# Kernel tuning notes

Hardware: AMD Instinct MI355X
Metric: run time of the kernel (lower is better)

The kernel has to match this reference:

```python
import jax, jax.numpy as jnp
import numpy as np


def _gcn_conv(x, W, b, src, dst, deg_inv_sqrt, n_nodes):
    # x: [N, Fin], W: [Fin, Fout]; edges (with self-loops): src, dst [E+N]
    h = x @ W  # [N, Fout]
    norm = deg_inv_sqrt[src] * deg_inv_sqrt[dst]  # [E+N]
    msgs = h[src] * norm[:, None]  # gather-multiply
    out = jax.ops.segment_sum(msgs, dst, num_segments=n_nodes)  # scatter-add
    return out + b


def setup_inputs() -> dict:
    key = jax.random.key(0)
    k1, k2, k3, k4 = jax.random.split(key, 4)
    N, E, FIN, HID, OUT = 100000, 3200000, 128, 32, 32
    x = jax.random.normal(k1, (N, FIN), dtype=jnp.float32)
    edge_index = jax.random.randint(k2, (2, E), 0, N, dtype=jnp.int64)
    W1 = jax.random.normal(k3, (FIN, HID), dtype=jnp.float32) * (1.0 / np.sqrt(FIN))
    b1 = jnp.zeros((HID,), dtype=jnp.float32)
    W2 = jax.random.normal(k4, (HID, OUT), dtype=jnp.float32) * (1.0 / np.sqrt(HID))
    b2 = jnp.zeros((OUT,), dtype=jnp.float32)
    return {"x": x, "edge_index": edge_index, "W1": W1, "b1": b1, "W2": W2, "b2": b2}


def reference(x, edge_index, W1, b1, W2, b2):
    n = x.shape[0]
    # GCNConv defaults: add self-loops, symmetric normalization D^-1/2 (A+I) D^-1/2
    loops = jnp.arange(n, dtype=edge_index.dtype)
    src = jnp.concatenate([edge_index[0], loops])
    dst = jnp.concatenate([edge_index[1], loops])
    deg = jax.ops.segment_sum(jnp.ones_like(dst, dtype=x.dtype), dst, num_segments=n)
    deg_inv_sqrt = jnp.where(deg > 0, jax.lax.rsqrt(jnp.maximum(deg, 1.0)), 0.0)
    h = jax.nn.relu(_gcn_conv(x, W1, b1, src, dst, deg_inv_sqrt, n))  # hidden layer + ReLU
    out = jax.nn.relu(_gcn_conv(h, W2, b2, src, dst, deg_inv_sqrt, n))  # last layer + last_activation relu
    return out
```

## Files before the change

kernel.cpp:

```cpp
#include <hip/hip_runtime.h>
#include <hip/hip_fp16.h>

#define FIN 128
#define HID 32
#define BSHIFT 8
#define BNODES 256
#define CHUNK 2048
#define NBMAX 512
#define CAPB 8960
#define G1ROWS 64
#define XPAD 4


__global__ __launch_bounds__(256) void chunk_sort_kernel(const int* __restrict__ src,
                                                         const int* __restrict__ dst,
                                                         int* __restrict__ ec,
                                                         unsigned short* __restrict__ offt,
                                                         int E, int nb) {
    __shared__ int hist[NBMAX];
    __shared__ int pref[NBMAX];
    __shared__ int wsum[128];
    __shared__ int sorted[CHUNK];
    int c = blockIdx.x, t = threadIdx.x;
    int beg = c * CHUNK;
    int cnt = min(CHUNK, E - beg);
    for (int i = t; i < nb; i += 256) hist[i] = 0;
    __syncthreads();
    int bk[8], ent[8];
    #pragma unroll
    for (int j = 0; j < 8; ++j) {
        int i = t + j * 256;
        if (i < cnt) {
            int d = dst[beg + i];
            bk[j]  = ((unsigned)d) >> BSHIFT;
            ent[j] = src[beg + i] | ((d & (BNODES - 1)) << 24);
            atomicAdd(&hist[bk[j]], 1);
        } else bk[j] = -1;
    }
    __syncthreads();
    if (t < 128) {
        int s = 0;
        #pragma unroll
        for (int j = 0; j < 4; ++j) {
            int idx = t * 4 + j;
            int v = (idx < nb) ? hist[idx] : 0;
            pref[idx] = s; s += v;
        }
        wsum[t] = s;
    }
    __syncthreads();
    if (t == 0) { int run = 0; for (int j = 0; j < 128; ++j) { int v = wsum[j]; wsum[j] = run; run += v; } }
    __syncthreads();
    for (int i = t; i < nb; i += 256) { int p = pref[i] + wsum[i >> 2]; pref[i] = p; hist[i] = p; }
    __syncthreads();
    #pragma unroll
    for (int j = 0; j < 8; ++j) {
        if (bk[j] >= 0) {
            int p = atomicAdd(&hist[bk[j]], 1);
            sorted[p] = ent[j];
        }
    }
    __syncthreads();
    for (int i = t; i < cnt; i += 256) ec[(size_t)c * CHUNK + i] = sorted[i];
    unsigned short* row = offt + (size_t)c * (nb + 1);
    for (int i = t; i < nb; i += 256) row[i] = (unsigned short)pref[i];
    if (t == 0) row[nb] = (unsigned short)cnt;
}


__global__ __launch_bounds__(1024) void bucket_build_kernel(const int* __restrict__ ec,
                                                            const unsigned short* __restrict__ offt,
                                                            int* __restrict__ entries,
                                                            float* __restrict__ dinv,
                                                            int* __restrict__ rowbeg,
                                                            int* __restrict__ rowcnt,
                                                            int n, int nb, int nchunks, int cap) {
    __shared__ int raw[CAPB];
    __shared__ int srt[CAPB];
    __shared__ int hist[BNODES];
    __shared__ int pref[BNODES];
    __shared__ int cursor[BNODES];
    __shared__ int wsum[64];
    __shared__ int nfill;
    int b = blockIdx.x, t = threadIdx.x;
    if (t < BNODES) hist[t] = 0;
    if (t == 0) nfill = 0;
    __syncthreads();
    for (int c = t; c < nchunks; c += 1024) {
        const unsigned short* row = offt + (size_t)c * (nb + 1);
        int s = row[b], e2 = row[b + 1];
        int m = e2 - s;
        if (m > 0) {
            int base = atomicAdd(&nfill, m);
            const int* p = ec + (size_t)c * CHUNK + s;
            for (int k = 0; k < m; ++k) {
                int e = p[k];
                if (base + k < CAPB) raw[base + k] = e;
                atomicAdd(&hist[((unsigned)e) >> 24], 1);
            }
        }
    }
    __syncthreads();
    int total = min(nfill, CAPB);
    if (t < 64) {
        int s = 0;
        #pragma unroll
        for (int j = 0; j < 4; ++j) { int v = hist[t * 4 + j]; pref[t * 4 + j] = s; s += v; }
        wsum[t] = s;
    }
    __syncthreads();
    if (t == 0) { int run = 0; for (int j = 0; j < 64; ++j) { int v = wsum[j]; wsum[j] = run; run += v; } }
    __syncthreads();
    if (t < BNODES) { int p = pref[t] + wsum[t >> 2]; pref[t] = p; cursor[t] = p; }
    __syncthreads();
    for (int i = t; i < total; i += 1024) {
        int e = raw[i];
        int p = atomicAdd(&cursor[((unsigned)e) >> 24], 1);
        srt[p] = e;
    }
    __syncthreads();
    int* ep = entries + (size_t)b * cap;
    for (int i = t; i < total; i += 1024) ep[i] = srt[i];
    int node = b * BNODES + t;
    if (t < BNODES && node < n) {
        int deg = hist[t];
        dinv[node]   = rsqrtf((float)deg + 1.0f);
        rowbeg[node] = b * cap + pref[t];
        rowcnt[node] = deg;
    }
}


__global__ __launch_bounds__(256) void gemm1_kernel(const float* __restrict__ x,
                                                    const float* __restrict__ W,
                                                    const float* __restrict__ dinv,
                                                    __half* __restrict__ h16, int n) {
    __shared__ float Ws[FIN * HID];
    int t = threadIdx.x;
    for (int i = t; i < FIN * HID; i += 256) Ws[i] = W[i];
    __syncthreads();
    int row0 = blockIdx.x * G1ROWS;
    int tr = t >> 3, tc = t & 7;
    int r0 = row0 + tr * 2, c0 = tc * 4;
    bool v0 = r0 < n, v1 = (r0 + 1) < n;
    const float* p0 = v0 ? &x[(size_t)r0 * FIN] : x;
    const float* p1 = v1 ? &x[(size_t)(r0 + 1) * FIN] : x;
    float4 a0 = make_float4(0.f, 0.f, 0.f, 0.f);
    float4 a1 = make_float4(0.f, 0.f, 0.f, 0.f);
    #pragma unroll 8
    for (int k4 = 0; k4 < FIN / 4; ++k4) {
        float4 xv0 = *(const float4*)&p0[k4 * 4];
        float4 xv1 = *(const float4*)&p1[k4 * 4];
        float4 w0 = *(const float4*)&Ws[(k4 * 4 + 0) * HID + c0];
        float4 w1 = *(const float4*)&Ws[(k4 * 4 + 1) * HID + c0];
        float4 w2 = *(const float4*)&Ws[(k4 * 4 + 2) * HID + c0];
        float4 w3 = *(const float4*)&Ws[(k4 * 4 + 3) * HID + c0];
        a0.x = fmaf(xv0.x, w0.x, a0.x); a0.y = fmaf(xv0.x, w0.y, a0.y);
        a0.z = fmaf(xv0.x, w0.z, a0.z); a0.w = fmaf(xv0.x, w0.w, a0.w);
        a0.x = fmaf(xv0.y, w1.x, a0.x); a0.y = fmaf(xv0.y, w1.y, a0.y);
        a0.z = fmaf(xv0.y, w1.z, a0.z); a0.w = fmaf(xv0.y, w1.w, a0.w);
        a0.x = fmaf(xv0.z, w2.x, a0.x); a0.y = fmaf(xv0.z, w2.y, a0.y);
        a0.z = fmaf(xv0.z, w2.z, a0.z); a0.w = fmaf(xv0.z, w2.w, a0.w);
        a0.x = fmaf(xv0.w, w3.x, a0.x); a0.y = fmaf(xv0.w, w3.y, a0.y);
        a0.z = fmaf(xv0.w, w3.z, a0.z); a0.w = fmaf(xv0.w, w3.w, a0.w);
        a1.x = fmaf(xv1.x, w0.x, a1.x); a1.y = fmaf(xv1.x, w0.y, a1.y);
        a1.z = fmaf(xv1.x, w0.z, a1.z); a1.w = fmaf(xv1.x, w0.w, a1.w);
        a1.x = fmaf(xv1.y, w1.x, a1.x); a1.y = fmaf(xv1.y, w1.y, a1.y);
        a1.z = fmaf(xv1.y, w1.z, a1.z); a1.w = fmaf(xv1.y, w1.w, a1.w);
        a1.x = fmaf(xv1.z, w2.x, a1.x); a1.y = fmaf(xv1.z, w2.y, a1.y);
        a1.z = fmaf(xv1.z, w2.z, a1.z); a1.w = fmaf(xv1.z, w2.w, a1.w);
        a1.x = fmaf(xv1.w, w3.x, a1.x); a1.y = fmaf(xv1.w, w3.y, a1.y);
        a1.z = fmaf(xv1.w, w3.z, a1.z); a1.w = fmaf(xv1.w, w3.w, a1.w);
    }
    #pragma unroll
    for (int rr = 0; rr < 2; ++rr) {
        int row = r0 + rr;
        float4 a = rr ? a1 : a0;
        float sc = (row < n) ? dinv[row] : 0.f;
        __half2 q0 = __floats2half2_rn(a.x * sc, a.y * sc);
        __half2 q1 = __floats2half2_rn(a.z * sc, a.w * sc);
        __half2* dstp = (__half2*)&h16[(size_t)row * HID + c0];
        dstp[0] = q0;
        dstp[1] = q1;
    }
}


__global__ __launch_bounds__(256) void gather_kernel(const int* __restrict__ entries,
                                                     const int* __restrict__ rowbeg,
                                                     const int* __restrict__ rowcnt,
                                                     const float* __restrict__ dinv,
                                                     const __half* __restrict__ h16,
                                                     const float* __restrict__ bias,
                                                     float* __restrict__ out, int n, int sent) {
    int t = threadIdx.x;
    int g = t >> 4, f = t & 15;
    int i = blockIdx.x * 16 + g;
    if (i >= n) return;
    float di = dinv[i];
    float s0, s1;
    {
        __half2 h = *(const __half2*)&h16[(size_t)i * HID + f * 2];
        float2 fp = __half22float2(h);
        s0 = fp.x; s1 = fp.y;
    }
    int beg = rowbeg[i], cnt = rowcnt[i];
    for (int base = 0; base < cnt; base += 16) {
        int idx = beg + base + f;
        int sv = ((base + f) < cnt) ? entries[idx] : sent;
        sv &= 0xFFFFFF;
        #pragma unroll
        for (int j0 = 0; j0 < 16; j0 += 8) {
            __half2 hv[8];
            #pragma unroll
            for (int j = 0; j < 8; ++j) {
                int e = __shfl(sv, j0 + j, 16);
                hv[j] = *(const __half2*)&h16[(size_t)e * HID + f * 2];
            }
            #pragma unroll
            for (int j = 0; j < 8; ++j) {
                s0 += __half2float(__low2half(hv[j]));
                s1 += __half2float(__high2half(hv[j]));
            }
        }
    }
    float2 b2 = *(const float2*)&bias[f * 2];
    float2 o;
    o.x = fmaxf(b2.x + di * s0, 0.f);
    o.y = fmaxf(b2.y + di * s1, 0.f);
    *(float2*)&out[(size_t)i * HID + f * 2] = o;
}


__global__ __launch_bounds__(256) void gemm2_kernel(const float* __restrict__ hin,
                                                    const float* __restrict__ W,
                                                    const float* __restrict__ dinv,
                                                    __half* __restrict__ h16, int n) {
    __shared__ float Ws[HID * HID];
    __shared__ float hs[G1ROWS][HID + XPAD];
    int t = threadIdx.x;
    for (int i = t; i < HID * HID; i += 256) Ws[i] = W[i];
    int row0 = blockIdx.x * G1ROWS;
    for (int idx = t; idx < G1ROWS * (HID / 4); idx += 256) {
        int r  = idx >> 3;
        int c4 = (idx & 7) * 4;
        int row = row0 + r;
        float4 v = (row < n) ? *(const float4*)&hin[(size_t)row * HID + c4]
                             : make_float4(0.f, 0.f, 0.f, 0.f);
        *(float4*)&hs[r][c4] = v;
    }
    __syncthreads();
    int tr = t >> 3, tc = t & 7;
    int r0 = tr * 2, c0 = tc * 4;
    float4 a0 = make_float4(0.f, 0.f, 0.f, 0.f);
    float4 a1 = make_float4(0.f, 0.f, 0.f, 0.f);
    #pragma unroll
    for (int k4 = 0; k4 < HID / 4; ++k4) {
        float4 xv0 = *(const float4*)&hs[r0][k4 * 4];
        float4 xv1 = *(const float4*)&hs[r0 + 1][k4 * 4];
        float4 w0 = *(const float4*)&Ws[(k4 * 4 + 0) * HID + c0];
        float4 w1 = *(const float4*)&Ws[(k4 * 4 + 1) * HID + c0];
        float4 w2 = *(const float4*)&Ws[(k4 * 4 + 2) * HID + c0];
        float4 w3 = *(const float4*)&Ws[(k4 * 4 + 3) * HID + c0];
        a0.x = fmaf(xv0.x, w0.x, a0.x); a0.y = fmaf(xv0.x, w0.y, a0.y);
        a0.z = fmaf(xv0.x, w0.z, a0.z); a0.w = fmaf(xv0.x, w0.w, a0.w);
        a0.x = fmaf(xv0.y, w1.x, a0.x); a0.y = fmaf(xv0.y, w1.y, a0.y);
        a0.z = fmaf(xv0.y, w1.z, a0.z); a0.w = fmaf(xv0.y, w1.w, a0.w);
        a0.x = fmaf(xv0.z, w2.x, a0.x); a0.y = fmaf(xv0.z, w2.y, a0.y);
        a0.z = fmaf(xv0.z, w2.z, a0.z); a0.w = fmaf(xv0.z, w2.w, a0.w);
        a0.x = fmaf(xv0.w, w3.x, a0.x); a0.y = fmaf(xv0.w, w3.y, a0.y);
        a0.z = fmaf(xv0.w, w3.z, a0.z); a0.w = fmaf(xv0.w, w3.w, a0.w);
        a1.x = fmaf(xv1.x, w0.x, a1.x); a1.y = fmaf(xv1.x, w0.y, a1.y);
        a1.z = fmaf(xv1.x, w0.z, a1.z); a1.w = fmaf(xv1.x, w0.w, a1.w);
        a1.x = fmaf(xv1.y, w1.x, a1.x); a1.y = fmaf(xv1.y, w1.y, a1.y);
        a1.z = fmaf(xv1.y, w1.z, a1.z); a1.w = fmaf(xv1.y, w1.w, a1.w);
        a1.x = fmaf(xv1.z, w2.x, a1.x); a1.y = fmaf(xv1.z, w2.y, a1.y);
        a1.z = fmaf(xv1.z, w2.z, a1.z); a1.w = fmaf(xv1.z, w2.w, a1.w);
        a1.x = fmaf(xv1.w, w3.x, a1.x); a1.y = fmaf(xv1.w, w3.y, a1.y);
        a1.z = fmaf(xv1.w, w3.z, a1.z); a1.w = fmaf(xv1.w, w3.w, a1.w);
    }
    #pragma unroll
    for (int rr = 0; rr < 2; ++rr) {
        int row = row0 + r0 + rr;
        float4 a = rr ? a1 : a0;
        float sc = (row < n) ? dinv[row] : 0.f;
        __half2 q0 = __floats2half2_rn(a.x * sc, a.y * sc);
        __half2 q1 = __floats2half2_rn(a.z * sc, a.w * sc);
        __half2* dstp = (__half2*)&h16[(size_t)row * HID + c0];
        dstp[0] = q0;
        dstp[1] = q1;
    }
}

extern "C" void kernel_launch(void* const* d_in, const int* in_sizes, int n_in,
                              void* d_out, int out_size, void* d_ws, size_t ws_size,
                              hipStream_t stream) {
    const float* x  = (const float*)d_in[0];
    const int*   ei = (const int*)d_in[1];
    const float* W1 = (const float*)d_in[2];
    const float* b1 = (const float*)d_in[3];
    const float* W2 = (const float*)d_in[4];
    const float* b2 = (const float*)d_in[5];
    float* out = (float*)d_out;

    int n = in_sizes[0] / FIN;
    int E = in_sizes[1] / 2;
    const int* src = ei;
    const int* dst = ei + E;

    int nb = (n + BNODES - 1) / BNODES;
    int nchunks = (E + CHUNK - 1) / CHUNK;
    int ggrid = (n + G1ROWS) / G1ROWS;
    int npad = ggrid * G1ROWS;
    int cap = CAPB;

    char* ws = (char*)d_ws;
    size_t off = 0;
    auto alloc = [&](size_t bytes) { char* p = ws + off; off += (bytes + 255) & ~(size_t)255; return p; };
    int*            ec      = (int*)alloc((size_t)nchunks * CHUNK * 4);
    unsigned short* offt    = (unsigned short*)alloc((size_t)nchunks * (nb + 1) * 2);
    int*            entries = (int*)alloc((size_t)nb * cap * 4);
    float*          dinv    = (float*)alloc((size_t)n * 4);
    int*            rowbeg  = (int*)alloc((size_t)n * 4);
    int*            rowcnt  = (int*)alloc((size_t)n * 4);
    float*          acc     = (float*)alloc((size_t)n * HID * 4);
    __half*         hh      = (__half*)alloc((size_t)npad * HID * 2);

    chunk_sort_kernel<<<nchunks, 256, 0, stream>>>(src, dst, ec, offt, E, nb);
    bucket_build_kernel<<<nb, 1024, 0, stream>>>(ec, offt, entries, dinv, rowbeg, rowcnt,
                                                 n, nb, nchunks, cap);

    gemm1_kernel<<<ggrid, 256, 0, stream>>>(x, W1, dinv, hh, n);
    gather_kernel<<<(n + 15) / 16, 256, 0, stream>>>(entries, rowbeg, rowcnt, dinv, hh, b1, acc, n, n);

    gemm2_kernel<<<ggrid, 256, 0, stream>>>(acc, W2, dinv, hh, n);
    gather_kernel<<<(n + 15) / 16, 256, 0, stream>>>(entries, rowbeg, rowcnt, dinv, hh, b2, out, n, n);
}
```

Measured before the change: 250.7 us.

## Widen gather to 16-byte row loads and use wave-shuffle prefix scans

The gather kernel now maps 4 lanes per node, each loading 8 fp16 features as one 16-byte vector, instead of 16 lanes each loading a 4-byte half2. This cuts the number of memory transactions per neighbour row and raises nodes per block from 16 to 64. The prefix scans in the sort and bucket kernels are replaced by a single-wave shuffle scan, which removes a serial thread-0 loop and two barriers. The bucket fill loop is also unrolled by four. The trade-off is more registers per thread in the gather, and fewer lanes per node to hide latency on high-degree nodes.

```diff
diff --git a/kernel.cpp b/kernel.cpp
--- a/kernel.cpp
+++ b/kernel.cpp
@@ -19,7 +19,6 @@
                                                          int E, int nb) {
     __shared__ int hist[NBMAX];
     __shared__ int pref[NBMAX];
-    __shared__ int wsum[128];
     __shared__ int sorted[CHUNK];
     int c = blockIdx.x, t = threadIdx.x;
     int beg = c * CHUNK;
@@ -38,20 +37,28 @@
         } else bk[j] = -1;
     }
     __syncthreads();
-    if (t < 128) {
+    if (t < 64) {
+        int v[8];
         int s = 0;
         #pragma unroll
-        for (int j = 0; j < 4; ++j) {
-            int idx = t * 4 + j;
-            int v = (idx < nb) ? hist[idx] : 0;
-            pref[idx] = s; s += v;
-        }
-        wsum[t] = s;
-    }
-    __syncthreads();
-    if (t == 0) { int run = 0; for (int j = 0; j < 128; ++j) { int v = wsum[j]; wsum[j] = run; run += v; } }
-    __syncthreads();
-    for (int i = t; i < nb; i += 256) { int p = pref[i] + wsum[i >> 2]; pref[i] = p; hist[i] = p; }
+        for (int j = 0; j < 8; ++j) {
+            int idx = t * 8 + j;
+            int h = (idx < nb) ? hist[idx] : 0;
+            v[j] = s; s += h;
+        }
+        int run = s;
+        #pragma unroll
+        for (int d = 1; d < 64; d <<= 1) {
+            int o = __shfl_up(run, d, 64);
+            if (t >= d) run += o;
+        }
+        int excl = run - s;
+        #pragma unroll
+        for (int j = 0; j < 8; ++j) {
+            int idx = t * 8 + j;
+            if (idx < nb) { int p = excl + v[j]; pref[idx] = p; hist[idx] = p; }
+        }
+    }
     __syncthreads();
     #pragma unroll
     for (int j = 0; j < 8; ++j) {
@@ -80,7 +87,6 @@
     __shared__ int hist[BNODES];
     __shared__ int pref[BNODES];
     __shared__ int cursor[BNODES];
-    __shared__ int wsum[64];
     __shared__ int nfill;
     int b = blockIdx.x, t = threadIdx.x;
     if (t < BNODES) hist[t] = 0;
@@ -93,7 +99,19 @@
         if (m > 0) {
             int base = atomicAdd(&nfill, m);
             const int* p = ec + (size_t)c * CHUNK + s;
-            for (int k = 0; k < m; ++k) {
+            int k = 0;
+            for (; k + 4 <= m; k += 4) {
+                int e0 = p[k], e1 = p[k + 1], e2v = p[k + 2], e3 = p[k + 3];
+                if (base + k + 0 < CAPB) raw[base + k + 0] = e0;
+                if (base + k + 1 < CAPB) raw[base + k + 1] = e1;
+                if (base + k + 2 < CAPB) raw[base + k + 2] = e2v;
+                if (base + k + 3 < CAPB) raw[base + k + 3] = e3;
+                atomicAdd(&hist[((unsigned)e0) >> 24], 1);
+                atomicAdd(&hist[((unsigned)e1) >> 24], 1);
+                atomicAdd(&hist[((unsigned)e2v) >> 24], 1);
+                atomicAdd(&hist[((unsigned)e3) >> 24], 1);
+            }
+            for (; k < m; ++k) {
                 int e = p[k];
                 if (base + k < CAPB) raw[base + k] = e;
                 atomicAdd(&hist[((unsigned)e) >> 24], 1);
@@ -103,15 +121,24 @@
     __syncthreads();
     int total = min(nfill, CAPB);
     if (t < 64) {
+        int v[4];
         int s = 0;
         #pragma unroll
-        for (int j = 0; j < 4; ++j) { int v = hist[t * 4 + j]; pref[t * 4 + j] = s; s += v; }
-        wsum[t] = s;
-    }
-    __syncthreads();
-    if (t == 0) { int run = 0; for (int j = 0; j < 64; ++j) { int v = wsum[j]; wsum[j] = run; run += v; } }
-    __syncthreads();
-    if (t < BNODES) { int p = pref[t] + wsum[t >> 2]; pref[t] = p; cursor[t] = p; }
+        for (int j = 0; j < 4; ++j) { v[j] = s; s += hist[t * 4 + j]; }
+        int run = s;
+        #pragma unroll
+        for (int d = 1; d < 64; d <<= 1) {
+            int o = __shfl_up(run, d, 64);
+            if (t >= d) run += o;
+        }
+        int excl = run - s;
+        #pragma unroll
+        for (int j = 0; j < 4; ++j) {
+            int idx = t * 4 + j;
+            int p = excl + v[j];
+            pref[idx] = p; cursor[idx] = p;
+        }
+    }
     __syncthreads();
     for (int i = t; i < total; i += 1024) {
         int e = raw[i];
@@ -194,41 +221,60 @@
                                                      const float* __restrict__ bias,
                                                      float* __restrict__ out, int n, int sent) {
     int t = threadIdx.x;
-    int g = t >> 4, f = t & 15;
-    int i = blockIdx.x * 16 + g;
+    int g = t >> 2, f = t & 3;
+    int i = blockIdx.x * 64 + g;
     if (i >= n) return;
     float di = dinv[i];
-    float s0, s1;
+    float a[8];
     {
-        __half2 h = *(const __half2*)&h16[(size_t)i * HID + f * 2];
-        float2 fp = __half22float2(h);
-        s0 = fp.x; s1 = fp.y;
+        float4 sv4 = *(const float4*)&h16[(size_t)i * HID + f * 8];
+        const __half2* sh = (const __half2*)&sv4;
+        #pragma unroll
+        for (int q = 0; q < 4; ++q) {
+            float2 fp = __half22float2(sh[q]);
+            a[2 * q] = fp.x; a[2 * q + 1] = fp.y;
+        }
     }
     int beg = rowbeg[i], cnt = rowcnt[i];
-    for (int base = 0; base < cnt; base += 16) {
-        int idx = beg + base + f;
-        int sv = ((base + f) < cnt) ? entries[idx] : sent;
-        sv &= 0xFFFFFF;
-        #pragma unroll
-        for (int j0 = 0; j0 < 16; j0 += 8) {
-            __half2 hv[8];
+    for (int base = 0; base < cnt; base += 8) {
+        int i0 = base + f, i1 = base + 4 + f;
+        int sv0 = (i0 < cnt) ? entries[beg + i0] : sent;
+        int sv1 = (i1 < cnt) ? entries[beg + i1] : sent;
+        sv0 &= 0xFFFFFF; sv1 &= 0xFFFFFF;
+        float4 hv[8];
+        #pragma unroll
+        for (int j = 0; j < 4; ++j) {
+            int e = __shfl(sv0, j, 4);
+            hv[j] = *(const float4*)&h16[(size_t)e * HID + f * 8];
+        }
+        #pragma unroll
+        for (int j = 0; j < 4; ++j) {
+            int e = __shfl(sv1, j, 4);
+            hv[4 + j] = *(const float4*)&h16[(size_t)e * HID + f * 8];
+        }
+        #pragma unroll
+        for (int j = 0; j < 8; ++j) {
+            const __half2* hp = (const __half2*)&hv[j];
             #pragma unroll
-            for (int j = 0; j < 8; ++j) {
-                int e = __shfl(sv, j0 + j, 16);
-                hv[j] = *(const __half2*)&h16[(size_t)e * HID + f * 2];
+            for (int q = 0; q < 4; ++q) {
+                float2 fp = __half22float2(hp[q]);
+                a[2 * q] += fp.x; a[2 * q + 1] += fp.y;
             }
-            #pragma unroll
-            for (int j = 0; j < 8; ++j) {
-                s0 += __half2float(__low2half(hv[j]));
-                s1 += __half2float(__high2half(hv[j]));
-            }
-        }
-    }
-    float2 b2 = *(const float2*)&bias[f * 2];
-    float2 o;
-    o.x = fmaxf(b2.x + di * s0, 0.f);
-    o.y = fmaxf(b2.y + di * s1, 0.f);
-    *(float2*)&out[(size_t)i * HID + f * 2] = o;
+        }
+    }
+    float4 b0 = *(const float4*)&bias[f * 8];
+    float4 b1 = *(const float4*)&bias[f * 8 + 4];
+    float4 o0, o1;
+    o0.x = fmaxf(b0.x + di * a[0], 0.f);
+    o0.y = fmaxf(b0.y + di * a[1], 0.f);
+    o0.z = fmaxf(b0.z + di * a[2], 0.f);
+    o0.w = fmaxf(b0.w + di * a[3], 0.f);
+    o1.x = fmaxf(b1.x + di * a[4], 0.f);
+    o1.y = fmaxf(b1.y + di * a[5], 0.f);
+    o1.z = fmaxf(b1.z + di * a[6], 0.f);
+    o1.w = fmaxf(b1.w + di * a[7], 0.f);
+    *(float4*)&out[(size_t)i * HID + f * 8] = o0;
+    *(float4*)&out[(size_t)i * HID + f * 8 + 4] = o1;
 }
 
 
@@ -331,8 +377,8 @@
                                                  n, nb, nchunks, cap);
 
     gemm1_kernel<<<ggrid, 256, 0, stream>>>(x, W1, dinv, hh, n);
-    gather_kernel<<<(n + 15) / 16, 256, 0, stream>>>(entries, rowbeg, rowcnt, dinv, hh, b1, acc, n, n);
+    gather_kernel<<<(n + 63) / 64, 256, 0, stream>>>(entries, rowbeg, rowcnt, dinv, hh, b1, acc, n, n);
 
     gemm2_kernel<<<ggrid, 256, 0, stream>>>(acc, W2, dinv, hh, n);
-    gather_kernel<<<(n + 15) / 16, 256, 0, stream>>>(entries, rowbeg, rowcnt, dinv, hh, b2, out, n, n);
-}
+    gather_kernel<<<(n + 63) / 64, 256, 0, stream>>>(entries, rowbeg, rowcnt, dinv, hh, b2, out, n, n);
+}
```

Result: no change. 254.2 us (+1.4%).
